# Kernel tuning notes

Measured on AMD Instinct MI355X. Metric: run time of the kernel, lower is better.

## Reference

```python
import jax, jax.numpy as jnp
import numpy as np

GRAPH_SIZE = 96
ROWS = 5
COLS = 4
BATCH = 2048


def setup_inputs() -> dict:
    key = jax.random.key(0)
    k1, k2 = jax.random.split(key)
    x = jax.random.normal(k1, (BATCH, GRAPH_SIZE, GRAPH_SIZE), dtype=jnp.float32)
    # coef: nn.Parameter zeros -> kaiming_normal_, i.e. N(0, sqrt(2/fan_in)), fan_in=COLS
    coef = jax.random.normal(k2, (ROWS, COLS), dtype=jnp.float32) * np.float32(np.sqrt(2.0 / COLS))
    return {"x": x, "coef": coef}


def _acoef(x, coef):
    """Batched version of ACoef.forward.

    Per sample: t_i = trace(x^(i+2)) for i in [0, rows); scalar out =
    sum_{i,j} coef[i,j] * t_i^(j+1) / (G*G)^(i+j+1).
    """
    rows, cols = coef.shape
    G = x.shape[-1]
    xr = x.reshape(-1, G, G)  # [B, G, G]
    a = jnp.matmul(xr, xr)    # x^2 == a_series[0]
    traces = []
    for i in range(rows):
        traces.append(jnp.einsum('bii->b', a))  # trace(x^(i+2))
        if i < rows - 1:
            a = jnp.matmul(xr, a)  # advance to x^(i+3)
    t = jnp.stack(traces, axis=1)  # [B, rows]
    numel = jnp.float32(G * G)
    jexp = jnp.arange(1, cols + 1, dtype=jnp.float32)  # j+1
    iexp = jnp.arange(rows, dtype=jnp.float32)         # i
    denom = numel ** (iexp[:, None] + jexp[None, :])   # numel^(i+j+1), [rows, cols]
    ret = (t[:, :, None] ** jexp[None, None, :]) / denom  # [B, rows, cols]
    return jnp.sum(coef[None, :, :] * ret, axis=(1, 2))   # [B]


def reference(x, coef):
    return _acoef(x, coef)
```

## Files before the change

kernel.cpp:

```cpp
#include <hip/hip_runtime.h>
#include <stdint.h>

#define G 96
#define GS (G*G)
#define ST 104
#define ARR (G*ST)
#define NT 256

typedef short bf16x8  __attribute__((ext_vector_type(8)));
typedef short short4v __attribute__((ext_vector_type(4)));
typedef float f32x4   __attribute__((ext_vector_type(4)));

__device__ __forceinline__ short f2bf(float f) {
  uint32_t u = __builtin_bit_cast(uint32_t, f);
  u += 0x7FFFu + ((u >> 16) & 1u);
  return (short)(u >> 16);
}
__device__ __forceinline__ float bf2f(short s) {
  uint32_t u = ((uint32_t)(uint16_t)s) << 16;
  return __builtin_bit_cast(float, u);
}

__device__ __forceinline__ void mm_phase(const short* __restrict__ P,
                                         const short* __restrict__ Q,
                                         int wm, int wn, int lr, int lq,
                                         f32x4 acc[3][3]) {
  #pragma unroll
  for (int ks = 0; ks < 3; ++ks) {
    const int k0 = ks*32 + lq*8;
    bf16x8 af[3], bg[3];
    #pragma unroll
    for (int i = 0; i < 3; ++i)
      af[i] = *reinterpret_cast<const bf16x8*>(&P[(wm + i*16 + lr)*ST + k0]);
    #pragma unroll
    for (int j = 0; j < 3; ++j)
      bg[j] = *reinterpret_cast<const bf16x8*>(&Q[(wn + j*16 + lr)*ST + k0]);
    #pragma unroll
    for (int i = 0; i < 3; ++i)
      #pragma unroll
      for (int j = 0; j < 3; ++j)
        acc[i][j] = __builtin_amdgcn_mfma_f32_16x16x32_bf16(af[i], bg[j], acc[i][j], 0, 0, 0);
  }
}

#define ZERO9(A) do { \
  _Pragma("unroll") for (int i_=0;i_<3;i_++) \
    _Pragma("unroll") for (int j_=0;j_<3;j_++) A[i_][j_] = (f32x4){0.f,0.f,0.f,0.f}; \
} while (0)

__global__ __launch_bounds__(NT, 4) void acoef_kernel(
    const float* __restrict__ x, const float* __restrict__ coef,
    float* __restrict__ out) {
  __shared__ short sm[2*ARR];
  __shared__ float red[4][8];
  __shared__ float cf[20];

  short* X  = sm;
  short* R1 = sm + ARR;

  const int tid  = threadIdx.x;
  const int b    = blockIdx.x;
  const int lane = tid & 63;
  const int w    = tid >> 6;
  const int wm   = (w >> 1) * 48;
  const int wn   = (w & 1)  * 48;
  const int lr   = lane & 15;
  const int lq   = lane >> 4;
  const int cr0  = lq * 4;

  if (tid < 20) cf[tid] = coef[tid];

  const float* xg = x + (size_t)b * GS;
  #pragma unroll
  for (int it = 0; it < 9; ++it) {
    int f = tid + it*NT;
    float4 v = reinterpret_cast<const float4*>(xg)[f];
    int row = f / 24, c4 = (f - row*24) * 4;
    short4v sv = {f2bf(v.x), f2bf(v.y), f2bf(v.z), f2bf(v.w)};
    *reinterpret_cast<short4v*>(&X[row*ST + c4]) = sv;
  }
  __syncthreads();

  #pragma unroll
  for (int it = 0; it < 9; ++it) {
    int u  = tid + it*NT;
    int r2 = u % 96, cb = (u / 96) * 4;
    short4v sv = { X[(cb+0)*ST + r2], X[(cb+1)*ST + r2],
                   X[(cb+2)*ST + r2], X[(cb+3)*ST + r2] };
    *reinterpret_cast<short4v*>(&R1[r2*ST + cb]) = sv;
  }
  __syncthreads();

  f32x4 accA[3][3];
  ZERO9(accA);
  mm_phase(X, R1, wm, wn, lr, lq, accA);

  float t0 = 0.f;
  #pragma unroll
  for (int i = 0; i < 3; ++i)
    #pragma unroll
    for (int j = 0; j < 3; ++j) {
      const int row0 = wm + i*16 + cr0, col = wn + j*16 + lr;
      #pragma unroll
      for (int r = 0; r < 4; ++r)
        if (row0 + r == col) t0 += accA[i][j][r];
    }
  __syncthreads();

  #pragma unroll
  for (int i = 0; i < 3; ++i)
    #pragma unroll
    for (int j = 0; j < 3; ++j) {
      const int row0 = wm + i*16 + cr0, col = wn + j*16 + lr;
      short4v sv = {f2bf(accA[i][j][0]), f2bf(accA[i][j][1]),
                    f2bf(accA[i][j][2]), f2bf(accA[i][j][3])};
      *reinterpret_cast<short4v*>(&R1[col*ST + row0]) = sv;
    }
  __syncthreads();

  f32x4 accB3[3][3];
  ZERO9(accB3);
  mm_phase(X, R1, wm, wn, lr, lq, accB3);

  float t1 = 0.f;
  #pragma unroll
  for (int i = 0; i < 3; ++i)
    #pragma unroll
    for (int j = 0; j < 3; ++j) {
      const int row0 = wm + i*16 + cr0, col = wn + j*16 + lr;
      #pragma unroll
      for (int r = 0; r < 4; ++r)
        if (row0 + r == col) t1 += accB3[i][j][r];
    }
  __syncthreads();

  #pragma unroll
  for (int i = 0; i < 3; ++i)
    #pragma unroll
    for (int j = 0; j < 3; ++j) {
      const int row0 = wm + i*16 + cr0, col = wn + j*16 + lr;
      #pragma unroll
      for (int r = 0; r < 4; ++r)
        X[(row0+r)*ST + col] = f2bf(accA[i][j][r]);
    }
  __syncthreads();

  short4v pr[3][3];
  float t3 = 0.f;
  #pragma unroll
  for (int i = 0; i < 3; ++i)
    #pragma unroll
    for (int j = 0; j < 3; ++j) {
      const int row0 = wm + i*16 + cr0, col = wn + j*16 + lr;
      pr[i][j] = *reinterpret_cast<const short4v*>(&X[col*ST + row0]);
      #pragma unroll
      for (int r = 0; r < 4; ++r)
        t3 += accB3[i][j][r] * bf2f(pr[i][j][r]);
    }

  f32x4 accA2[3][3];
  ZERO9(accA2);
  mm_phase(X, R1, wm, wn, lr, lq, accA2);

  float t2 = 0.f, t4 = 0.f;
  #pragma unroll
  for (int i = 0; i < 3; ++i)
    #pragma unroll
    for (int j = 0; j < 3; ++j) {
      const int row0 = wm + i*16 + cr0, col = wn + j*16 + lr;
      #pragma unroll
      for (int r = 0; r < 4; ++r) {
        float v = accA2[i][j][r];
        if (row0 + r == col) t2 += v;
        t4 += v * bf2f(pr[i][j][r]);
      }
    }

  #pragma unroll
  for (int off = 32; off > 0; off >>= 1) {
    t0 += __shfl_down(t0, off, 64);
    t1 += __shfl_down(t1, off, 64);
    t2 += __shfl_down(t2, off, 64);
    t3 += __shfl_down(t3, off, 64);
    t4 += __shfl_down(t4, off, 64);
  }
  if (lane == 0) {
    red[w][0]=t0; red[w][1]=t1; red[w][2]=t2; red[w][3]=t3; red[w][4]=t4;
  }
  __syncthreads();
  if (tid == 0) {
    float T[5];
    #pragma unroll
    for (int k = 0; k < 5; ++k) T[k] = red[0][k]+red[1][k]+red[2][k]+red[3][k];
    const float inv = 1.0f / (float)GS;
    float o = 0.f, pi = 1.f;
    #pragma unroll
    for (int i = 0; i < 5; ++i) {
      float u = T[i] * inv;
      float up = u;
      #pragma unroll
      for (int j = 0; j < 4; ++j) { o += cf[i*4+j] * up * pi; up *= u; }
      pi *= inv;
    }
    out[b] = o;
  }
}

extern "C" void kernel_launch(void* const* d_in, const int* in_sizes, int n_in,
                              void* d_out, int out_size, void* d_ws, size_t ws_size,
                              hipStream_t stream) {
  const float* x    = (const float*)d_in[0];
  const float* coef = (const float*)d_in[1];
  float* out        = (float*)d_out;
  const int batch   = in_sizes[0] / GS;
  acoef_kernel<<<batch, NT, 0, stream>>>(x, coef, out);
}
```

Before: 31.48 us.

## Reorder power-trace chain to use products with the resident operand

Restructures how the five traces are derived across the three bf16 MFMA matmuls. Traces of X^3 and X^4 now come from elementwise products of the current accumulator with the transposed operand already in LDS, which removes the separate write-back of X^2 over the X buffer. The global load is widened to write 8 bf16 values per LDS store instead of 4. The launch-bounds occupancy hint drops from 4 to 3, giving the compiler more registers but allowing fewer resident blocks. The new trace reads are scalar 16-bit LDS loads, and tr(X^4) is now formed from bf16-rounded values, which slightly changes numerics.

New measurement: 33.75 us. 1.07x slower.

```diff
diff --git a/kernel.cpp b/kernel.cpp
--- a/kernel.cpp
+++ b/kernel.cpp
@@ -20,6 +20,12 @@
   uint32_t u = ((uint32_t)(uint16_t)s) << 16;
   return __builtin_bit_cast(float, u);
 }
+__device__ __forceinline__ float unlo(uint32_t u) {
+  return __builtin_bit_cast(float, u << 16);
+}
+__device__ __forceinline__ float unhi(uint32_t u) {
+  return __builtin_bit_cast(float, u & 0xffff0000u);
+}
 
 __device__ __forceinline__ void mm_phase(const short* __restrict__ P,
                                          const short* __restrict__ Q,
@@ -48,7 +54,7 @@
     _Pragma("unroll") for (int j_=0;j_<3;j_++) A[i_][j_] = (f32x4){0.f,0.f,0.f,0.f}; \
 } while (0)
 
-__global__ __launch_bounds__(NT, 4) void acoef_kernel(
+__global__ __launch_bounds__(NT, 3) void acoef_kernel(
     const float* __restrict__ x, const float* __restrict__ coef,
     float* __restrict__ out) {
   __shared__ short sm[2*ARR];
@@ -72,12 +78,16 @@
 
   const float* xg = x + (size_t)b * GS;
   #pragma unroll
-  for (int it = 0; it < 9; ++it) {
-    int f = tid + it*NT;
-    float4 v = reinterpret_cast<const float4*>(xg)[f];
-    int row = f / 24, c4 = (f - row*24) * 4;
-    short4v sv = {f2bf(v.x), f2bf(v.y), f2bf(v.z), f2bf(v.w)};
-    *reinterpret_cast<short4v*>(&X[row*ST + c4]) = sv;
+  for (int it = 0; it < 5; ++it) {
+    int c = tid + it*NT;
+    if (c < GS/8) {
+      float4 v0 = reinterpret_cast<const float4*>(xg)[2*c];
+      float4 v1 = reinterpret_cast<const float4*>(xg)[2*c+1];
+      int row = c / 12, col8 = (c - row*12) * 8;
+      bf16x8 sv = { f2bf(v0.x), f2bf(v0.y), f2bf(v0.z), f2bf(v0.w),
+                    f2bf(v1.x), f2bf(v1.y), f2bf(v1.z), f2bf(v1.w) };
+      *reinterpret_cast<bf16x8*>(&X[row*ST + col8]) = sv;
+    }
   }
   __syncthreads();
 
@@ -91,78 +101,11 @@
   }
   __syncthreads();
 
-  f32x4 accA[3][3];
-  ZERO9(accA);
-  mm_phase(X, R1, wm, wn, lr, lq, accA);
-
-  float t0 = 0.f;
-  #pragma unroll
-  for (int i = 0; i < 3; ++i)
-    #pragma unroll
-    for (int j = 0; j < 3; ++j) {
-      const int row0 = wm + i*16 + cr0, col = wn + j*16 + lr;
-      #pragma unroll
-      for (int r = 0; r < 4; ++r)
-        if (row0 + r == col) t0 += accA[i][j][r];
-    }
-  __syncthreads();
-
-  #pragma unroll
-  for (int i = 0; i < 3; ++i)
-    #pragma unroll
-    for (int j = 0; j < 3; ++j) {
-      const int row0 = wm + i*16 + cr0, col = wn + j*16 + lr;
-      short4v sv = {f2bf(accA[i][j][0]), f2bf(accA[i][j][1]),
-                    f2bf(accA[i][j][2]), f2bf(accA[i][j][3])};
-      *reinterpret_cast<short4v*>(&R1[col*ST + row0]) = sv;
-    }
-  __syncthreads();
-
-  f32x4 accB3[3][3];
-  ZERO9(accB3);
-  mm_phase(X, R1, wm, wn, lr, lq, accB3);
-
-  float t1 = 0.f;
-  #pragma unroll
-  for (int i = 0; i < 3; ++i)
-    #pragma unroll
-    for (int j = 0; j < 3; ++j) {
-      const int row0 = wm + i*16 + cr0, col = wn + j*16 + lr;
-      #pragma unroll
-      for (int r = 0; r < 4; ++r)
-        if (row0 + r == col) t1 += accB3[i][j][r];
-    }
-  __syncthreads();
-
-  #pragma unroll
-  for (int i = 0; i < 3; ++i)
-    #pragma unroll
-    for (int j = 0; j < 3; ++j) {
-      const int row0 = wm + i*16 + cr0, col = wn + j*16 + lr;
-      #pragma unroll
-      for (int r = 0; r < 4; ++r)
-        X[(row0+r)*ST + col] = f2bf(accA[i][j][r]);
-    }
-  __syncthreads();
-
-  short4v pr[3][3];
-  float t3 = 0.f;
-  #pragma unroll
-  for (int i = 0; i < 3; ++i)
-    #pragma unroll
-    for (int j = 0; j < 3; ++j) {
-      const int row0 = wm + i*16 + cr0, col = wn + j*16 + lr;
-      pr[i][j] = *reinterpret_cast<const short4v*>(&X[col*ST + row0]);
-      #pragma unroll
-      for (int r = 0; r < 4; ++r)
-        t3 += accB3[i][j][r] * bf2f(pr[i][j][r]);
-    }
-
-  f32x4 accA2[3][3];
-  ZERO9(accA2);
-  mm_phase(X, R1, wm, wn, lr, lq, accA2);
-
-  float t2 = 0.f, t4 = 0.f;
+  f32x4 acc1[3][3];
+  ZERO9(acc1);
+  mm_phase(X, R1, wm, wn, lr, lq, acc1);
+
+  float t0 = 0.f, t1 = 0.f;
   #pragma unroll
   for (int i = 0; i < 3; ++i)
     #pragma unroll
@@ -170,10 +113,72 @@
       const int row0 = wm + i*16 + cr0, col = wn + j*16 + lr;
       #pragma unroll
       for (int r = 0; r < 4; ++r) {
-        float v = accA2[i][j][r];
-        if (row0 + r == col) t2 += v;
-        t4 += v * bf2f(pr[i][j][r]);
+        float a = acc1[i][j][r];
+        if (row0 + r == col) t0 += a;
+        t1 += a * bf2f(R1[(row0+r)*ST + col]);
       }
+    }
+  __syncthreads();
+
+  #pragma unroll
+  for (int i = 0; i < 3; ++i)
+    #pragma unroll
+    for (int j = 0; j < 3; ++j) {
+      const int row0 = wm + i*16 + cr0, col = wn + j*16 + lr;
+      short4v sv = {f2bf(acc1[i][j][0]), f2bf(acc1[i][j][1]),
+                    f2bf(acc1[i][j][2]), f2bf(acc1[i][j][3])};
+      *reinterpret_cast<short4v*>(&R1[col*ST + row0]) = sv;
+    }
+  __syncthreads();
+
+  f32x4 acc2[3][3];
+  ZERO9(acc2);
+  mm_phase(X, R1, wm, wn, lr, lq, acc2);
+
+  float t2 = 0.f, t3 = 0.f;
+  uint32_t pr[3][3][2];
+  #pragma unroll
+  for (int i = 0; i < 3; ++i)
+    #pragma unroll
+    for (int j = 0; j < 3; ++j) {
+      const int row0 = wm + i*16 + cr0, col = wn + j*16 + lr;
+      uint16_t p0 = (uint16_t)R1[(row0+0)*ST + col];
+      uint16_t p1 = (uint16_t)R1[(row0+1)*ST + col];
+      uint16_t p2 = (uint16_t)R1[(row0+2)*ST + col];
+      uint16_t p3 = (uint16_t)R1[(row0+3)*ST + col];
+      uint32_t q0 = (uint32_t)p0 | ((uint32_t)p1 << 16);
+      uint32_t q1 = (uint32_t)p2 | ((uint32_t)p3 << 16);
+      pr[i][j][0] = q0; pr[i][j][1] = q1;
+      t2 += acc1[i][j][0]*unlo(q0) + acc1[i][j][1]*unhi(q0)
+          + acc1[i][j][2]*unlo(q1) + acc1[i][j][3]*unhi(q1);
+      t3 += acc2[i][j][0]*unlo(q0) + acc2[i][j][1]*unhi(q0)
+          + acc2[i][j][2]*unlo(q1) + acc2[i][j][3]*unhi(q1);
+    }
+  __syncthreads();
+
+  #pragma unroll
+  for (int i = 0; i < 3; ++i)
+    #pragma unroll
+    for (int j = 0; j < 3; ++j) {
+      const int row0 = wm + i*16 + cr0, col = wn + j*16 + lr;
+      short4v sv = {f2bf(acc2[i][j][0]), f2bf(acc2[i][j][1]),
+                    f2bf(acc2[i][j][2]), f2bf(acc2[i][j][3])};
+      *reinterpret_cast<short4v*>(&R1[col*ST + row0]) = sv;
+    }
+  __syncthreads();
+
+  f32x4 acc3[3][3];
+  ZERO9(acc3);
+  mm_phase(X, R1, wm, wn, lr, lq, acc3);
+
+  float t4 = 0.f;
+  #pragma unroll
+  for (int i = 0; i < 3; ++i)
+    #pragma unroll
+    for (int j = 0; j < 3; ++j) {
+      uint32_t q0 = pr[i][j][0], q1 = pr[i][j][1];
+      t4 += acc3[i][j][0]*unlo(q0) + acc3[i][j][1]*unhi(q0)
+          + acc3[i][j][2]*unlo(q1) + acc3[i][j][3]*unhi(q1);
     }
 
   #pragma unroll
```
